# Performance work log

Hardware: AMD Instinct MI355X
Metric: run time of the kernel (lower is better)

Reference implementation:

```python
import jax, jax.numpy as jnp
import numpy as np

NUM_EMBEDDINGS = 8192
EMBEDDING_DIM = 64
COMMITMENT_COST = 0.25


def setup_inputs() -> dict:
    key = jax.random.key(0)
    kx, ke = jax.random.split(key)
    x = jax.random.normal(kx, (32, 1024, EMBEDDING_DIM), dtype=jnp.float32)
    embeddings = jax.random.normal(ke, (NUM_EMBEDDINGS, EMBEDDING_DIM), dtype=jnp.float32)
    return {"x": x, "embeddings": embeddings}


def reference(x, embeddings):
    d = embeddings.shape[1]
    flat_x = x.reshape(-1, d)  # [N, D]
    # squared euclidean distances (argmin identical to cdist argmin):
    d2 = (
        jnp.sum(flat_x * flat_x, axis=-1, keepdims=True)
        - 2.0 * flat_x @ embeddings.T
        + jnp.sum(embeddings * embeddings, axis=-1)
    )
    encoding_indices = jnp.argmin(d2, axis=1)  # [N]
    quantized = embeddings[encoding_indices].reshape(x.shape)
    codebook_loss = jnp.mean((jax.lax.stop_gradient(quantized) - x) ** 2)
    commitment_loss = COMMITMENT_COST * jnp.mean((quantized - jax.lax.stop_gradient(x)) ** 2)
    loss = codebook_loss + commitment_loss
    # straight-through estimator
    quantized_st = x + jax.lax.stop_gradient(quantized - x)
    return quantized_st, loss, encoding_indices
```

## Files before the change

kernel.cpp:

```cpp
#include <hip/hip_runtime.h>
#include <hip/hip_bf16.h>
#include <float.h>

#define N_ROWS 32768
#define DIMS   64
#define K_EMB  8192
#define NT     (K_EMB / 16)
#define NTH    (NT / 2)
#define TSTAGE 8
#define NSTAGE (NTH / TSTAGE)
#define GAP_THR 1.5e-3f

typedef __attribute__((ext_vector_type(8))) short s8v;
typedef __attribute__((ext_vector_type(4))) float f4v;
typedef __attribute__((ext_vector_type(4))) int   i4v;

#define WS_EFRAG 0
#define WS_EN2   (2 * 1024 * 1024)
#define WS_IDX   (WS_EN2 + K_EMB * 4)
#define WS_KEY   (WS_IDX + N_ROWS * 4)
#define WS_BH    (WS_KEY + N_ROWS * 8)
#define WS_SH    (WS_BH + 2 * N_ROWS * 4)
#define WS_CH    (WS_SH + 2 * N_ROWS * 4)
#define WS_CTL   (WS_CH + 2 * N_ROWS * 4)
#define WS_WL    (WS_CTL + 16)

#define OUT_LOSS (N_ROWS * DIMS)
#define OUT_IDX  (N_ROWS * DIMS + 1)

__device__ inline short bfh(float v) {
    __hip_bfloat16 h = __float2bfloat16(v);
    return __builtin_bit_cast(short, h);
}
__device__ inline float bff(short s) {
    __hip_bfloat16 h = __builtin_bit_cast(__hip_bfloat16, s);
    return __bfloat162float(h);
}

__global__ void vq_prep(const float* __restrict__ emb, short* __restrict__ efrag,
                        float* __restrict__ en2) {
    int gid = blockIdx.x * 256 + threadIdx.x;
    int t = gid >> 6, lane = gid & 63;
    int m = lane & 15, q = lane >> 4;
    const float* er = emb + (size_t)(t * 16 + m) * DIMS;
    s8v hi0, lo0, hi1, lo1;
    float ss = 0.f;
#pragma unroll
    for (int j = 0; j < 8; ++j) {
        float v0 = er[q * 8 + j];
        float v1 = er[32 + q * 8 + j];
        ss += v0 * v0 + v1 * v1;
        short h0 = bfh(v0); lo0[j] = bfh(v0 - bff(h0)); hi0[j] = h0;
        short h1 = bfh(v1); lo1[j] = bfh(v1 - bff(h1)); hi1[j] = h1;
    }
    s8v* base = (s8v*)efrag + (size_t)t * 4 * 64;
    base[0 * 64 + lane] = hi0;
    base[1 * 64 + lane] = hi1;
    base[2 * 64 + lane] = lo0;
    base[3 * 64 + lane] = lo1;
    ss += __shfl_xor(ss, 16, 64);
    ss += __shfl_xor(ss, 32, 64);
    if (q == 0) en2[t * 16 + m] = -0.5f * ss;
}

__global__ __launch_bounds__(256, 2) void vq_phase1(
    const float* __restrict__ x, const short* __restrict__ efrag,
    const float* __restrict__ en2,
    float* __restrict__ bh, float* __restrict__ sh, int* __restrict__ ch) {
    __shared__ __align__(16) char lds[2][TSTAGE * 4096];
    int tid = threadIdx.x, wid = tid >> 6, lane = tid & 63;
    int m = lane & 15, q = lane >> 4;
    int kh = blockIdx.y;
    int row0 = blockIdx.x * 128 + wid * 32;

    s8v ahi[2][2], alo[2][2];
#pragma unroll
    for (int g = 0; g < 2; ++g) {
        const float* xr = x + (size_t)(row0 + g * 16 + m) * DIMS + q * 8;
#pragma unroll
        for (int j = 0; j < 8; ++j) {
            float v0 = xr[j], v1 = xr[32 + j];
            short h0 = bfh(v0); alo[g][0][j] = bfh(v0 - bff(h0)); ahi[g][0][j] = h0;
            short h1 = bfh(v1); alo[g][1][j] = bfh(v1 - bff(h1)); ahi[g][1][j] = h1;
        }
    }

    float best[2][4], sec[2][4];
    int bc[2][4];
#pragma unroll
    for (int g = 0; g < 2; ++g)
#pragma unroll
        for (int r = 0; r < 4; ++r) { best[g][r] = -FLT_MAX; sec[g][r] = -FLT_MAX; bc[g][r] = 0; }

    const char* gsrc = (const char*)efrag + (size_t)kh * NTH * 4096;

#pragma unroll
    for (int i = 0; i < 8; ++i)
        __builtin_amdgcn_global_load_lds(
            (const __attribute__((address_space(1))) void*)(gsrc + i * 4096 + tid * 16),
            (__attribute__((address_space(3))) void*)(&lds[0][i * 4096 + tid * 16]),
            16, 0, 0);
    __syncthreads();

    for (int s = 0; s < NSTAGE; ++s) {
        int pb = s & 1;
        if (s + 1 < NSTAGE) {
            const char* gn = gsrc + (size_t)(s + 1) * TSTAGE * 4096;
#pragma unroll
            for (int i = 0; i < 8; ++i)
                __builtin_amdgcn_global_load_lds(
                    (const __attribute__((address_space(1))) void*)(gn + i * 4096 + tid * 16),
                    (__attribute__((address_space(3))) void*)(&lds[pb ^ 1][i * 4096 + tid * 16]),
                    16, 0, 0);
        }
        const i4v* B = (const i4v*)(lds[pb]);
        int tg0 = kh * NTH + s * TSTAGE;
        const float* ep = en2 + (size_t)tg0 * 16 + m;
#pragma unroll
        for (int tt = 0; tt < TSTAGE; ++tt) {
            i4v b0 = B[tt * 256 + 0 * 64 + lane];
            i4v b1 = B[tt * 256 + 1 * 64 + lane];
            i4v b2 = B[tt * 256 + 2 * 64 + lane];
            i4v b3 = B[tt * 256 + 3 * 64 + lane];
            float c0 = ep[tt * 16];
            int cidx = (tg0 + tt) * 16 + m;
#pragma unroll
            for (int g = 0; g < 2; ++g) {
                f4v acc = {c0, c0, c0, c0};
                acc = __builtin_amdgcn_mfma_f32_16x16x32_bf16(ahi[g][0], __builtin_bit_cast(s8v, b0), acc, 0, 0, 0);
                acc = __builtin_amdgcn_mfma_f32_16x16x32_bf16(ahi[g][1], __builtin_bit_cast(s8v, b1), acc, 0, 0, 0);
                acc = __builtin_amdgcn_mfma_f32_16x16x32_bf16(ahi[g][0], __builtin_bit_cast(s8v, b2), acc, 0, 0, 0);
                acc = __builtin_amdgcn_mfma_f32_16x16x32_bf16(ahi[g][1], __builtin_bit_cast(s8v, b3), acc, 0, 0, 0);
                acc = __builtin_amdgcn_mfma_f32_16x16x32_bf16(alo[g][0], __builtin_bit_cast(s8v, b0), acc, 0, 0, 0);
                acc = __builtin_amdgcn_mfma_f32_16x16x32_bf16(alo[g][1], __builtin_bit_cast(s8v, b1), acc, 0, 0, 0);
#pragma unroll
                for (int r = 0; r < 4; ++r) {
                    float v = acc[r];
                    bool gt = v > best[g][r];
                    sec[g][r]  = fmaxf(sec[g][r], fminf(v, best[g][r]));
                    best[g][r] = fmaxf(best[g][r], v);
                    bc[g][r]   = gt ? cidx : bc[g][r];
                }
            }
        }
        __syncthreads();
    }

#pragma unroll
    for (int g = 0; g < 2; ++g)
#pragma unroll
    for (int r = 0; r < 4; ++r) {
        float b = best[g][r], s = sec[g][r];
        int c = bc[g][r];
#pragma unroll
        for (int off = 1; off < 16; off <<= 1) {
            float ob = __shfl_xor(b, off, 64);
            float os = __shfl_xor(s, off, 64);
            int   oc = __shfl_xor(c, off, 64);
            float nb = fmaxf(b, ob);
            float ns = fmaxf(fminf(b, ob), fmaxf(s, os));
            bool take = (ob > b) || (ob == b && oc < c);
            c = take ? oc : c;
            b = nb; s = ns;
        }
        if (m == 0) {
            int o = kh * N_ROWS + row0 + g * 16 + q * 4 + r;
            bh[o] = b; sh[o] = s; ch[o] = c;
        }
    }
}

__global__ void vq_merge(const float* __restrict__ bh, const float* __restrict__ sh,
                         const int* __restrict__ ch, int* __restrict__ idx_buf,
                         unsigned long long* __restrict__ key8,
                         int* __restrict__ wl, int* __restrict__ wl_count) {
    int row = blockIdx.x * 256 + threadIdx.x;
    float b0 = bh[row], b1 = bh[N_ROWS + row];
    float s0 = sh[row], s1 = sh[N_ROWS + row];
    int   c0 = ch[row], c1 = ch[N_ROWS + row];
    float nb = fmaxf(b0, b1);
    float ns = fmaxf(fminf(b0, b1), fmaxf(s0, s1));
    int c = (b1 > b0) ? c1 : c0;
    idx_buf[row] = c;
    key8[row] = 0ULL;
    if (nb - ns < GAP_THR) {
        int pos = atomicAdd(wl_count, 1);
        wl[pos] = row;
    }
}

__global__ __launch_bounds__(256) void vq_fixup(
    const float* __restrict__ x, const float* __restrict__ emb,
    const float* __restrict__ en2, unsigned long long* __restrict__ key8,
    const int* __restrict__ wl, const int* __restrict__ wl_count) {
    __shared__ float4 sx[16];
    __shared__ float sbf[4];
    __shared__ int   sbc[4];
    int tid = threadIdx.x, wid = tid >> 6, lane = tid & 63;
    int cnt = *wl_count;
    for (int wi = blockIdx.x; wi < cnt * 8; wi += gridDim.x) {
        int row = wl[wi >> 3];
        int cbase = (wi & 7) * (K_EMB / 8);
        if (tid < 16) sx[tid] = ((const float4*)(x + (size_t)row * DIMS))[tid];
        __syncthreads();
        float bf_ = -FLT_MAX;
        int bc_ = 0;
        for (int c = cbase + tid; c < cbase + K_EMB / 8; c += 256) {
            const float4* er = (const float4*)(emb + (size_t)c * DIMS);
            float d = 0.f;
#pragma unroll
            for (int qq = 0; qq < 16; ++qq) {
                float4 e = er[qq];
                float4 xx = sx[qq];
                d += e.x * xx.x + e.y * xx.y + e.z * xx.z + e.w * xx.w;
            }
            float f = d + en2[c];
            if (f > bf_) { bf_ = f; bc_ = c; }
        }
#pragma unroll
        for (int off = 1; off < 64; off <<= 1) {
            float of = __shfl_xor(bf_, off, 64);
            int   oc = __shfl_xor(bc_, off, 64);
            if (of > bf_ || (of == bf_ && oc < bc_)) { bf_ = of; bc_ = oc; }
        }
        if (lane == 0) { sbf[wid] = bf_; sbc[wid] = bc_; }
        __syncthreads();
        if (tid == 0) {
            float b = sbf[0]; int c = sbc[0];
#pragma unroll
            for (int i = 1; i < 4; ++i)
                if (sbf[i] > b || (sbf[i] == b && sbc[i] < c)) { b = sbf[i]; c = sbc[i]; }
            unsigned int u = __float_as_uint(b);
            unsigned int sb = ((int)u < 0) ? ~u : (u | 0x80000000u);
            unsigned long long key = ((unsigned long long)sb << 32) | (unsigned int)(~c);
            atomicMax(&key8[row], key);
        }
        __syncthreads();
    }
}

__global__ void vq_gather(const float* __restrict__ x, const float* __restrict__ emb,
                          const int* __restrict__ idx_buf,
                          const unsigned long long* __restrict__ key8,
                          float* __restrict__ out, double* __restrict__ loss_acc) {
    int row = blockIdx.x * blockDim.x + threadIdx.x;
    unsigned long long k = key8[row];
    int idx = k ? (int)(~(unsigned int)k) : idx_buf[row];
    const float4* ev = (const float4*)(emb + (size_t)idx * DIMS);
    const float4* xv = (const float4*)(x + (size_t)row * DIMS);
    float4* ov = (float4*)(out + (size_t)row * DIMS);
    float s = 0.f;
#pragma unroll
    for (int qq = 0; qq < 16; ++qq) {
        float4 ee = ev[qq];
        float4 xx = xv[qq];
        float dx = ee.x - xx.x, dy = ee.y - xx.y, dz = ee.z - xx.z, dw = ee.w - xx.w;
        s += dx * dx + dy * dy + dz * dz + dw * dw;
        ov[qq] = ee;
    }
#pragma unroll
    for (int off = 32; off > 0; off >>= 1) s += __shfl_down(s, off, 64);
    if ((threadIdx.x & 63) == 0) atomicAdd(loss_acc, (double)s);
    out[OUT_IDX + row] = (float)idx;
}

__global__ void vq_loss(const double* __restrict__ acc, float* __restrict__ out) {
    out[OUT_LOSS] = (float)(1.25 * (*acc) / (double)(N_ROWS * DIMS));
}

extern "C" void kernel_launch(void* const* d_in, const int* in_sizes, int n_in,
                              void* d_out, int out_size, void* d_ws, size_t ws_size,
                              hipStream_t stream) {
    const float* x   = (const float*)d_in[0];
    const float* emb = (const float*)d_in[1];
    float* out = (float*)d_out;
    char*  ws  = (char*)d_ws;

    short* efrag   = (short*)(ws + WS_EFRAG);
    float* en2     = (float*)(ws + WS_EN2);
    int*   idx_buf = (int*)(ws + WS_IDX);
    unsigned long long* key8 = (unsigned long long*)(ws + WS_KEY);
    float* bhb     = (float*)(ws + WS_BH);
    float* shb     = (float*)(ws + WS_SH);
    int*   chb     = (int*)(ws + WS_CH);
    double* loss_acc = (double*)(ws + WS_CTL);
    int*   wl_count  = (int*)(ws + WS_CTL + 8);
    int*   wl        = (int*)(ws + WS_WL);

    hipMemsetAsync(ws + WS_CTL, 0, 16, stream);

    vq_prep<<<(NT * 64) / 256, 256, 0, stream>>>(emb, efrag, en2);
    vq_phase1<<<dim3(N_ROWS / 128, 2), 256, 0, stream>>>(x, efrag, en2, bhb, shb, chb);
    vq_merge<<<N_ROWS / 256, 256, 0, stream>>>(bhb, shb, chb, idx_buf, key8, wl, wl_count);
    vq_fixup<<<2048, 256, 0, stream>>>(x, emb, en2, key8, wl, wl_count);
    vq_gather<<<N_ROWS / 256, 256, 0, stream>>>(x, emb, idx_buf, key8, out, loss_acc);
    vq_loss<<<1, 1, 0, stream>>>(loss_acc, out);
}
```

Before: 200.7 us.

## Switch distance GEMM to 32x32x16 MFMA with index packed into mantissa

The phase-1 distance kernel moves from 16x16x32 to 32x32x16 bf16 MFMA tiles, and the codebook fragments are re-laid out to match. The tile index is now packed into the low 7 mantissa bits of each score, and fmed3 tracks the second-best value. This removes the per-element index select and cuts instruction overhead in the argmax loop. Packing perturbs the scores, so the near-tie gap threshold is raised, which sends more rows to the exact fixup path. The separate loss kernel is also dropped: the last gather block finalizes the loss through an atomic completion counter, saving one launch.

```diff
diff --git a/kernel.cpp b/kernel.cpp
--- a/kernel.cpp
+++ b/kernel.cpp
@@ -5,15 +5,15 @@
 #define N_ROWS 32768
 #define DIMS   64
 #define K_EMB  8192
-#define NT     (K_EMB / 16)
-#define NTH    (NT / 2)
-#define TSTAGE 8
-#define NSTAGE (NTH / TSTAGE)
-#define GAP_THR 1.5e-3f
-
-typedef __attribute__((ext_vector_type(8))) short s8v;
-typedef __attribute__((ext_vector_type(4))) float f4v;
-typedef __attribute__((ext_vector_type(4))) int   i4v;
+#define NT32   (K_EMB / 32)
+#define NTH32  (NT32 / 2)
+#define TSTAGE 4
+#define NSTAGE (NTH32 / TSTAGE)
+#define GAP_THR 4.0e-3f
+
+typedef __attribute__((ext_vector_type(8)))  short s8v;
+typedef __attribute__((ext_vector_type(16))) float f16v;
+typedef __attribute__((ext_vector_type(4)))  int   i4v;
 
 #define WS_EFRAG 0
 #define WS_EN2   (2 * 1024 * 1024)
@@ -41,58 +41,57 @@
                         float* __restrict__ en2) {
     int gid = blockIdx.x * 256 + threadIdx.x;
     int t = gid >> 6, lane = gid & 63;
-    int m = lane & 15, q = lane >> 4;
-    const float* er = emb + (size_t)(t * 16 + m) * DIMS;
-    s8v hi0, lo0, hi1, lo1;
+    int n = lane & 31, q2 = lane >> 5;
+    const float* er = emb + (size_t)(t * 32 + n) * DIMS + q2 * 8;
+    s8v hi[4], lo[4];
     float ss = 0.f;
 #pragma unroll
-    for (int j = 0; j < 8; ++j) {
-        float v0 = er[q * 8 + j];
-        float v1 = er[32 + q * 8 + j];
-        ss += v0 * v0 + v1 * v1;
-        short h0 = bfh(v0); lo0[j] = bfh(v0 - bff(h0)); hi0[j] = h0;
-        short h1 = bfh(v1); lo1[j] = bfh(v1 - bff(h1)); hi1[j] = h1;
-    }
-    s8v* base = (s8v*)efrag + (size_t)t * 4 * 64;
-    base[0 * 64 + lane] = hi0;
-    base[1 * 64 + lane] = hi1;
-    base[2 * 64 + lane] = lo0;
-    base[3 * 64 + lane] = lo1;
-    ss += __shfl_xor(ss, 16, 64);
+    for (int kc = 0; kc < 4; ++kc) {
+#pragma unroll
+        for (int j = 0; j < 8; ++j) {
+            float v = er[kc * 16 + j];
+            ss += v * v;
+            short h = bfh(v); lo[kc][j] = bfh(v - bff(h)); hi[kc][j] = h;
+        }
+    }
+    s8v* base = (s8v*)efrag + (size_t)t * 8 * 64;
+#pragma unroll
+    for (int kc = 0; kc < 4; ++kc) {
+        base[kc * 64 + lane]       = hi[kc];
+        base[(4 + kc) * 64 + lane] = lo[kc];
+    }
     ss += __shfl_xor(ss, 32, 64);
-    if (q == 0) en2[t * 16 + m] = -0.5f * ss;
+    if (q2 == 0) en2[t * 32 + n] = -0.5f * ss;
 }
 
 __global__ __launch_bounds__(256, 2) void vq_phase1(
     const float* __restrict__ x, const short* __restrict__ efrag,
     const float* __restrict__ en2,
     float* __restrict__ bh, float* __restrict__ sh, int* __restrict__ ch) {
-    __shared__ __align__(16) char lds[2][TSTAGE * 4096];
+    __shared__ __align__(16) char lds[2][TSTAGE * 8192];
     int tid = threadIdx.x, wid = tid >> 6, lane = tid & 63;
-    int m = lane & 15, q = lane >> 4;
+    int n = lane & 31, q2 = lane >> 5;
     int kh = blockIdx.y;
     int row0 = blockIdx.x * 128 + wid * 32;
 
-    s8v ahi[2][2], alo[2][2];
-#pragma unroll
-    for (int g = 0; g < 2; ++g) {
-        const float* xr = x + (size_t)(row0 + g * 16 + m) * DIMS + q * 8;
-#pragma unroll
-        for (int j = 0; j < 8; ++j) {
-            float v0 = xr[j], v1 = xr[32 + j];
-            short h0 = bfh(v0); alo[g][0][j] = bfh(v0 - bff(h0)); ahi[g][0][j] = h0;
-            short h1 = bfh(v1); alo[g][1][j] = bfh(v1 - bff(h1)); ahi[g][1][j] = h1;
-        }
-    }
-
-    float best[2][4], sec[2][4];
-    int bc[2][4];
-#pragma unroll
-    for (int g = 0; g < 2; ++g)
-#pragma unroll
-        for (int r = 0; r < 4; ++r) { best[g][r] = -FLT_MAX; sec[g][r] = -FLT_MAX; bc[g][r] = 0; }
-
-    const char* gsrc = (const char*)efrag + (size_t)kh * NTH * 4096;
+    s8v ahi[4], alo[4];
+    {
+        const float* xr = x + (size_t)(row0 + n) * DIMS + q2 * 8;
+#pragma unroll
+        for (int kc = 0; kc < 4; ++kc)
+#pragma unroll
+            for (int j = 0; j < 8; ++j) {
+                float v = xr[kc * 16 + j];
+                short h = bfh(v); alo[kc][j] = bfh(v - bff(h)); ahi[kc][j] = h;
+            }
+    }
+
+    float best[16], sec[16];
+#pragma unroll
+    for (int r = 0; r < 16; ++r) { best[r] = -FLT_MAX; sec[r] = -FLT_MAX; }
+
+    const char* gsrc = (const char*)efrag + (size_t)kh * NTH32 * 8192;
+    const float* ep = en2 + kh * (K_EMB / 2) + n;
 
 #pragma unroll
     for (int i = 0; i < 8; ++i)
@@ -105,7 +104,7 @@
     for (int s = 0; s < NSTAGE; ++s) {
         int pb = s & 1;
         if (s + 1 < NSTAGE) {
-            const char* gn = gsrc + (size_t)(s + 1) * TSTAGE * 4096;
+            const char* gn = gsrc + (size_t)(s + 1) * TSTAGE * 8192;
 #pragma unroll
             for (int i = 0; i < 8; ++i)
                 __builtin_amdgcn_global_load_lds(
@@ -114,58 +113,61 @@
                     16, 0, 0);
         }
         const i4v* B = (const i4v*)(lds[pb]);
-        int tg0 = kh * NTH + s * TSTAGE;
-        const float* ep = en2 + (size_t)tg0 * 16 + m;
-#pragma unroll
-        for (int tt = 0; tt < TSTAGE; ++tt) {
-            i4v b0 = B[tt * 256 + 0 * 64 + lane];
-            i4v b1 = B[tt * 256 + 1 * 64 + lane];
-            i4v b2 = B[tt * 256 + 2 * 64 + lane];
-            i4v b3 = B[tt * 256 + 3 * 64 + lane];
-            float c0 = ep[tt * 16];
-            int cidx = (tg0 + tt) * 16 + m;
-#pragma unroll
-            for (int g = 0; g < 2; ++g) {
-                f4v acc = {c0, c0, c0, c0};
-                acc = __builtin_amdgcn_mfma_f32_16x16x32_bf16(ahi[g][0], __builtin_bit_cast(s8v, b0), acc, 0, 0, 0);
-                acc = __builtin_amdgcn_mfma_f32_16x16x32_bf16(ahi[g][1], __builtin_bit_cast(s8v, b1), acc, 0, 0, 0);
-                acc = __builtin_amdgcn_mfma_f32_16x16x32_bf16(ahi[g][0], __builtin_bit_cast(s8v, b2), acc, 0, 0, 0);
-                acc = __builtin_amdgcn_mfma_f32_16x16x32_bf16(ahi[g][1], __builtin_bit_cast(s8v, b3), acc, 0, 0, 0);
-                acc = __builtin_amdgcn_mfma_f32_16x16x32_bf16(alo[g][0], __builtin_bit_cast(s8v, b0), acc, 0, 0, 0);
-                acc = __builtin_amdgcn_mfma_f32_16x16x32_bf16(alo[g][1], __builtin_bit_cast(s8v, b1), acc, 0, 0, 0);
-#pragma unroll
-                for (int r = 0; r < 4; ++r) {
-                    float v = acc[r];
-                    bool gt = v > best[g][r];
-                    sec[g][r]  = fmaxf(sec[g][r], fminf(v, best[g][r]));
-                    best[g][r] = fmaxf(best[g][r], v);
-                    bc[g][r]   = gt ? cidx : bc[g][r];
-                }
+        int tg0 = s * TSTAGE;
+#pragma unroll
+        for (int tp = 0; tp < TSTAGE; tp += 2) {
+            i4v bb0[8], bb1[8];
+#pragma unroll
+            for (int f = 0; f < 8; ++f) {
+                bb0[f] = B[(tp + 0) * 512 + f * 64 + lane];
+                bb1[f] = B[(tp + 1) * 512 + f * 64 + lane];
             }
+            float c00 = ep[(tg0 + tp + 0) * 32];
+            float c01 = ep[(tg0 + tp + 1) * 32];
+            f16v acc0, acc1;
+#pragma unroll
+            for (int r = 0; r < 16; ++r) { acc0[r] = c00; acc1[r] = c01; }
+#define STEP(Aop, F) \
+            acc0 = __builtin_amdgcn_mfma_f32_32x32x16_bf16(Aop, __builtin_bit_cast(s8v, bb0[F]), acc0, 0, 0, 0); \
+            acc1 = __builtin_amdgcn_mfma_f32_32x32x16_bf16(Aop, __builtin_bit_cast(s8v, bb1[F]), acc1, 0, 0, 0);
+            STEP(ahi[0], 0) STEP(ahi[1], 1) STEP(ahi[2], 2) STEP(ahi[3], 3)
+            STEP(ahi[0], 4) STEP(ahi[1], 5) STEP(ahi[2], 6) STEP(ahi[3], 7)
+            STEP(alo[0], 0) STEP(alo[1], 1) STEP(alo[2], 2) STEP(alo[3], 3)
+#undef STEP
+            int tb0 = (~(tg0 + tp + 0)) & 0x7F;
+            int tb1 = (~(tg0 + tp + 1)) & 0x7F;
+#pragma unroll
+            for (int r = 0; r < 16; ++r) {
+                float v0 = __int_as_float((__float_as_int(acc0[r]) & 0xFFFFFF80) | tb0);
+                sec[r]  = __builtin_amdgcn_fmed3f(v0, best[r], sec[r]);
+                best[r] = fmaxf(best[r], v0);
+                float v1 = __int_as_float((__float_as_int(acc1[r]) & 0xFFFFFF80) | tb1);
+                sec[r]  = __builtin_amdgcn_fmed3f(v1, best[r], sec[r]);
+                best[r] = fmaxf(best[r], v1);
+            }
         }
         __syncthreads();
     }
 
 #pragma unroll
-    for (int g = 0; g < 2; ++g)
-#pragma unroll
-    for (int r = 0; r < 4; ++r) {
-        float b = best[g][r], s = sec[g][r];
-        int c = bc[g][r];
-#pragma unroll
-        for (int off = 1; off < 16; off <<= 1) {
+    for (int r = 0; r < 16; ++r) {
+        float b = best[r], s2 = sec[r];
+        int c = ((~__float_as_int(b)) & 0x7F) * 32 + n;
+#pragma unroll
+        for (int off = 1; off < 32; off <<= 1) {
             float ob = __shfl_xor(b, off, 64);
-            float os = __shfl_xor(s, off, 64);
+            float os = __shfl_xor(s2, off, 64);
             int   oc = __shfl_xor(c, off, 64);
             float nb = fmaxf(b, ob);
-            float ns = fmaxf(fminf(b, ob), fmaxf(s, os));
+            float ns = fmaxf(fminf(b, ob), fmaxf(s2, os));
             bool take = (ob > b) || (ob == b && oc < c);
             c = take ? oc : c;
-            b = nb; s = ns;
-        }
-        if (m == 0) {
-            int o = kh * N_ROWS + row0 + g * 16 + q * 4 + r;
-            bh[o] = b; sh[o] = s; ch[o] = c;
+            b = nb; s2 = ns;
+        }
+        if (n == 0) {
+            int row = row0 + (r & 3) + 8 * (r >> 2) + 4 * q2;
+            int o = kh * N_ROWS + row;
+            bh[o] = b; sh[o] = s2; ch[o] = kh * (K_EMB / 2) + c;
         }
     }
 }
@@ -242,7 +244,8 @@
 __global__ void vq_gather(const float* __restrict__ x, const float* __restrict__ emb,
                           const int* __restrict__ idx_buf,
                           const unsigned long long* __restrict__ key8,
-                          float* __restrict__ out, double* __restrict__ loss_acc) {
+                          float* __restrict__ out, double* __restrict__ loss_acc,
+                          int* __restrict__ done_ctr) {
     int row = blockIdx.x * blockDim.x + threadIdx.x;
     unsigned long long k = key8[row];
     int idx = k ? (int)(~(unsigned int)k) : idx_buf[row];
@@ -262,10 +265,15 @@
     for (int off = 32; off > 0; off >>= 1) s += __shfl_down(s, off, 64);
     if ((threadIdx.x & 63) == 0) atomicAdd(loss_acc, (double)s);
     out[OUT_IDX + row] = (float)idx;
-}
-
-__global__ void vq_loss(const double* __restrict__ acc, float* __restrict__ out) {
-    out[OUT_LOSS] = (float)(1.25 * (*acc) / (double)(N_ROWS * DIMS));
+    __syncthreads();
+    if (threadIdx.x == 0) {
+        __threadfence();
+        int d = atomicAdd(done_ctr, 1);
+        if (d == (int)gridDim.x - 1) {
+            double tot = atomicAdd(loss_acc, 0.0);
+            out[OUT_LOSS] = (float)(1.25 * tot / (double)(N_ROWS * DIMS));
+        }
+    }
 }
 
 extern "C" void kernel_launch(void* const* d_in, const int* in_sizes, int n_in,
@@ -285,14 +293,14 @@
     int*   chb     = (int*)(ws + WS_CH);
     double* loss_acc = (double*)(ws + WS_CTL);
     int*   wl_count  = (int*)(ws + WS_CTL + 8);
+    int*   done_ctr  = (int*)(ws + WS_CTL + 12);
     int*   wl        = (int*)(ws + WS_WL);
 
     hipMemsetAsync(ws + WS_CTL, 0, 16, stream);
 
-    vq_prep<<<(NT * 64) / 256, 256, 0, stream>>>(emb, efrag, en2);
+    vq_prep<<<(NT32 * 64) / 256, 256, 0, stream>>>(emb, efrag, en2);
     vq_phase1<<<dim3(N_ROWS / 128, 2), 256, 0, stream>>>(x, efrag, en2, bhb, shb, chb);
     vq_merge<<<N_ROWS / 256, 256, 0, stream>>>(bhb, shb, chb, idx_buf, key8, wl, wl_count);
     vq_fixup<<<2048, 256, 0, stream>>>(x, emb, en2, key8, wl, wl_count);
-    vq_gather<<<N_ROWS / 256, 256, 0, stream>>>(x, emb, idx_buf, key8, out, loss_acc);
-    vq_loss<<<1, 1, 0, stream>>>(loss_acc, out);
-}
+    vq_gather<<<N_ROWS / 256, 256, 0, stream>>>(x, emb, idx_buf, key8, out, loss_acc, done_ctr);
+}
```

After: 226.1 us. 12.6% more time.
